# Kernel optimization log

Measured on AMD Instinct MI355X. Metric: run time of the kernel, lower is better.

Reference implementation:

```python
import jax, jax.numpy as jnp
import numpy as np

B, T, D = 2048, 200, 64
H1, H2 = 128, 64
NEG_INF = jnp.float32(-(2.0**32) + 1.0)


def setup_inputs() -> dict:
    key = jax.random.key(0)
    ks = jax.random.split(key, 10)
    query = jax.random.normal(ks[0], (B, D), dtype=jnp.float32)
    k = jax.random.normal(ks[1], (B, T, D), dtype=jnp.float32)
    v = jax.random.normal(ks[2], (B, T, D), dtype=jnp.float32)
    mask = jax.random.randint(ks[3], (B, T), 0, 2, dtype=jnp.int32)
    # Deep_layer params: concat width 4*D -> H1 -> H2 -> 1
    s1 = 1.0 / np.sqrt(4 * D)
    s2 = 1.0 / np.sqrt(H1)
    s3 = 1.0 / np.sqrt(H2)
    W1 = jax.random.normal(ks[4], (4 * D, H1), dtype=jnp.float32) * s1
    b1 = jnp.zeros((H1,), dtype=jnp.float32)
    W2 = jax.random.normal(ks[5], (H1, H2), dtype=jnp.float32) * s2
    b2 = jnp.zeros((H2,), dtype=jnp.float32)
    Wo = jax.random.normal(ks[6], (H2, 1), dtype=jnp.float32) * s3
    bo = jnp.zeros((1,), dtype=jnp.float32)
    return {"query": query, "key": k, "value": v, "mask": mask,
            "W1": W1, "b1": b1, "W2": W2, "b2": b2, "Wo": Wo, "bo": bo}


def reference(query, key, value, mask, W1, b1, W2, b2, Wo, bo):
    b, t, d = key.shape
    q = jnp.broadcast_to(query[:, None, :], (b, t, d))          # tile query over T
    emb = jnp.concatenate([q, key, q - key, q * key], axis=-1)  # [B,T,4D]
    h = jax.nn.relu(jnp.einsum('btf,fh->bth', emb, W1) + b1)    # [B,T,H1]
    h = jax.nn.relu(jnp.einsum('bth,hk->btk', h, W2) + b2)      # [B,T,H2]
    score = (jnp.einsum('btk,ko->bto', h, Wo) + bo)[..., 0]     # [B,T]
    score = jnp.where(mask == 0, NEG_INF, score)
    attn = jax.nn.softmax(score, axis=-1)                       # [B,T]
    out = jnp.einsum('bt,btd->bd', attn, value)                 # [B,D]
    return out
```

## Files before the change

### kernel.cpp

```cpp
#include <hip/hip_runtime.h>
#include <hip/hip_bf16.h>
#include <cstdint>
#include <cstddef>

#define NB 2048
#define NT 200
#define ND 64
#define NH1 128
#define NH2 64
#define NTILES 7
#define NTP 224

typedef __bf16 bf16x8 __attribute__((ext_vector_type(8)));
typedef float f32x4 __attribute__((ext_vector_type(4)));

#define MFMA16(A, Bv, C) __builtin_amdgcn_mfma_f32_16x16x32_bf16((A), (Bv), (C), 0, 0, 0)

union BF8u { __bf16 b[8]; bf16x8 v; uint4 u4; };

template<int N>
__device__ __forceinline__ float row_ror_add(float v) {
    int r = __builtin_amdgcn_update_dpp(0, __builtin_bit_cast(int, v),
                                        0x120 | N, 0xF, 0xF, false);
    return v + __builtin_bit_cast(float, r);
}

__global__ void prep_kernel(const float* __restrict__ W1, const float* __restrict__ W2,
                            float* __restrict__ Qp, float* __restrict__ AbT,
                            float* __restrict__ PT, __bf16* __restrict__ W2t) {
    int tid = blockIdx.x * blockDim.x + threadIdx.x;
    if (tid < 64 * NH1) {
        int c = tid >> 7, j = tid & 127;
        Qp[tid] = W1[c * NH1 + j] + W1[(128 + c) * NH1 + j];
        int jj = tid >> 6, cc = tid & 63;
        AbT[tid] = W1[(64 + cc) * NH1 + jj] - W1[(128 + cc) * NH1 + jj];
        PT[tid]  = W1[(192 + cc) * NH1 + jj];
        int j2 = tid >> 7, k = tid & 127;
        W2t[tid] = (__bf16)W2[k * NH2 + j2];
    }
}

__global__ __launch_bounds__(256, 4)
void attn_main(const float* __restrict__ query, const float* __restrict__ key,
               const float* __restrict__ value, const int* __restrict__ mask,
               const float* __restrict__ b1, const float* __restrict__ b2,
               const float* __restrict__ Wo,
               const float* __restrict__ Qp, const float* __restrict__ AbT,
               const float* __restrict__ PT, const __bf16* __restrict__ W2t,
               float* __restrict__ out)
{
    __shared__ __align__(16) char smem[30976];
    auto KHI0 = (__bf16(*)[72])(smem);
    auto KHI1 = (__bf16(*)[72])(smem + 4608);
    auto H10  = (__bf16(*)[136])(smem + 9216);
    auto H11  = (__bf16(*)[136])(smem + 17920);
    auto SP   = (float(*)[NTP])(smem + 26624);
    float* QS  = (float*)(smem + 30208);
    float* QHS = (float*)(smem + 30464);
    float* SCORES = (float*)(smem);
    auto REDS = (float(*)[72])(smem + 9216);

    const int b = blockIdx.x;
    const int tid = threadIdx.x;
    const int lane = tid & 63;
    const int wave = tid >> 6;
    const int jn = lane & 15;
    const int g4 = lane >> 4;
    const int g8 = g4 * 8;

    const int r_st = tid >> 3;
    const int c0   = (tid & 7) * 8;
    const float* kp_base = key + (size_t)b * NT * ND + c0;
    float4 pf0, pf1;

    auto load_tile = [&](int t0) {
        int t = t0 + r_st;
        t = t < NT ? t : NT - 1;
        const float* kp = kp_base + (size_t)t * ND;
        pf0 = *(const float4*)(kp);
        pf1 = *(const float4*)(kp + 4);
    };

    load_tile(0);

    if (tid < ND) QS[tid] = query[(size_t)b * ND + tid];
    int mk = 0;
    if (tid < NT) mk = mask[(size_t)b * NT + tid];
    __syncthreads();

    if (tid < NH1) {
        float a = b1[tid];
        #pragma unroll 8
        for (int c = 0; c < ND; ++c) a = fmaf(QS[c], Qp[c * NH1 + tid], a);
        QHS[tid] = a;
    }

    bf16x8 g1_bhi[2][2], g1_blo[2][2];
    const int jown = wave * 32;
    #pragma unroll
    for (int n = 0; n < 2; ++n) {
        const int j = jown + n * 16 + jn;
        #pragma unroll
        for (int kk = 0; kk < 2; ++kk) {
            const float* ab = AbT + j * ND + kk * 32 + g8;
            const float* pt = PT  + j * ND + kk * 32 + g8;
            float4 a0 = *(const float4*)ab, a1 = *(const float4*)(ab + 4);
            float4 p0 = *(const float4*)pt, p1 = *(const float4*)(pt + 4);
            const float va[8] = {a0.x,a0.y,a0.z,a0.w,a1.x,a1.y,a1.z,a1.w};
            const float vp[8] = {p0.x,p0.y,p0.z,p0.w,p1.x,p1.y,p1.z,p1.w};
            BF8u vh, vl;
            #pragma unroll
            for (int e = 0; e < 8; ++e) {
                const int c = kk * 32 + g8 + e;
                float v = fmaf(QS[c], vp[e], va[e]);
                __bf16 hi = (__bf16)v;
                vh.b[e] = hi;
                vl.b[e] = (__bf16)(v - (float)hi);
            }
            g1_bhi[n][kk] = vh.v;
            g1_blo[n][kk] = vl.v;
        }
    }
    bf16x8 g2_w[4];
    {
        const int j2 = wave * 16 + jn;
        #pragma unroll
        for (int kk = 0; kk < 4; ++kk)
            g2_w[kk] = *(const bf16x8*)(W2t + j2 * NH1 + kk * 32 + g8);
    }
    __syncthreads();
    const float qh0 = QHS[jown + jn];
    const float qh1 = QHS[jown + 16 + jn];
    const float b2j = b2[wave * 16 + jn];
    const float woj = Wo[wave * 16 + jn];

    f32x4 accc[2][2];
    for (int ti = 0; ti <= NTILES; ++ti) {
        __bf16 (*KCUR)[72]   = (ti & 1) ? KHI1 : KHI0;
        __bf16 (*H1CUR)[136] = ((ti - 1) & 1) ? H11 : H10;

        if (ti < NTILES) {
            const float vals[8] = {pf0.x, pf0.y, pf0.z, pf0.w, pf1.x, pf1.y, pf1.z, pf1.w};
            BF8u ph;
            #pragma unroll
            for (int i = 0; i < 8; ++i) ph.b[i] = (__bf16)vals[i];
            *(uint4*)(&KCUR[r_st][c0]) = ph.u4;
        }
        if (ti > 0) {
            #pragma unroll
            for (int mt = 0; mt < 2; ++mt)
            #pragma unroll
            for (int n = 0; n < 2; ++n) {
                const float qhj = n ? qh1 : qh0;
                const int j = jown + n * 16 + jn;
                #pragma unroll
                for (int r = 0; r < 4; ++r)
                    H1CUR[mt * 16 + g4 * 4 + r][j] =
                        (__bf16)fmaxf(accc[mt][n][r] + qhj, 0.f);
            }
        }
        __syncthreads();

        if (ti + 1 < NTILES) load_tile((ti + 1) * 32);

        if (ti < NTILES) {
            #pragma unroll
            for (int mt = 0; mt < 2; ++mt) {
                const int arow = mt * 16 + jn;
                const bf16x8 a0 = *(const bf16x8*)(&KCUR[arow][g8]);
                const bf16x8 a1 = *(const bf16x8*)(&KCUR[arow][32 + g8]);
                #pragma unroll
                for (int n = 0; n < 2; ++n) {
                    f32x4 ac = {0.f, 0.f, 0.f, 0.f};
                    ac = MFMA16(a0, g1_bhi[n][0], ac);
                    ac = MFMA16(a1, g1_bhi[n][1], ac);
                    ac = MFMA16(a0, g1_blo[n][0], ac);
                    ac = MFMA16(a1, g1_blo[n][1], ac);
                    accc[mt][n] = ac;
                }
            }
        }
        if (ti > 0) {
            const int t0 = (ti - 1) * 32;
            #pragma unroll
            for (int mt = 0; mt < 2; ++mt) {
                const int arow = mt * 16 + jn;
                const bf16x8 h0v = *(const bf16x8*)(&H1CUR[arow][g8]);
                const bf16x8 h1v = *(const bf16x8*)(&H1CUR[arow][32 + g8]);
                const bf16x8 h2v = *(const bf16x8*)(&H1CUR[arow][64 + g8]);
                const bf16x8 h3v = *(const bf16x8*)(&H1CUR[arow][96 + g8]);
                f32x4 cA = {0.f,0.f,0.f,0.f}, cB = {0.f,0.f,0.f,0.f};
                cA = MFMA16(h0v, g2_w[0], cA);
                cB = MFMA16(h1v, g2_w[1], cB);
                cA = MFMA16(h2v, g2_w[2], cA);
                cB = MFMA16(h3v, g2_w[3], cB);
                #pragma unroll
                for (int r = 0; r < 4; ++r) {
                    float v = fmaxf(cA[r] + cB[r] + b2j, 0.f) * woj;
                    v = row_ror_add<8>(v);
                    v = row_ror_add<4>(v);
                    v = row_ror_add<2>(v);
                    v = row_ror_add<1>(v);
                    if (jn == 0) SP[wave][t0 + mt * 16 + g4 * 4 + r] = v;
                }
            }
        }
    }
    __syncthreads();

    if (tid < NTP) {
        const float sc = SP[0][tid] + SP[1][tid] + SP[2][tid] + SP[3][tid];
        SCORES[tid] = (tid < NT && mk != 0) ? __expf(sc) : 0.f;
    }
    __syncthreads();

    {
        const int tg = tid >> 4;
        const int dq = tid & 15;
        const float* vbase = value + (size_t)b * NT * ND + dq * 4;
        float oa0 = 0.f, oa1 = 0.f, oa2 = 0.f, oa3 = 0.f, den = 0.f;
        for (int t = tg; t < NT; t += 16) {
            const float e = SCORES[t];
            const float4 v4 = *(const float4*)(vbase + (size_t)t * ND);
            oa0 = fmaf(e, v4.x, oa0); oa1 = fmaf(e, v4.y, oa1);
            oa2 = fmaf(e, v4.z, oa2); oa3 = fmaf(e, v4.w, oa3);
            den += e;
        }
        REDS[tg][dq*4+0] = oa0; REDS[tg][dq*4+1] = oa1;
        REDS[tg][dq*4+2] = oa2; REDS[tg][dq*4+3] = oa3;
        if (dq == 0) REDS[tg][64] = den;
    }
    __syncthreads();

    if (tid < ND) {
        float s = 0.f, den = 0.f;
        #pragma unroll
        for (int g = 0; g < 16; ++g) { s += REDS[g][tid]; den += REDS[g][64]; }
        out[(size_t)b * ND + tid] = s / den;
    }
}

extern "C" void kernel_launch(void* const* d_in, const int* in_sizes, int n_in,
                              void* d_out, int out_size, void* d_ws, size_t ws_size,
                              hipStream_t stream) {
    const float* query = (const float*)d_in[0];
    const float* key   = (const float*)d_in[1];
    const float* value = (const float*)d_in[2];
    const int*   maskp = (const int*)d_in[3];
    const float* W1    = (const float*)d_in[4];
    const float* b1    = (const float*)d_in[5];
    const float* W2    = (const float*)d_in[6];
    const float* b2    = (const float*)d_in[7];
    const float* Wo    = (const float*)d_in[8];
    float* out = (float*)d_out;

    float* Qp  = (float*)d_ws;
    float* AbT = Qp + 64 * NH1;
    float* PT  = AbT + NH1 * ND;
    __bf16* W2t = (__bf16*)(PT + NH1 * ND);

    prep_kernel<<<32, 256, 0, stream>>>(W1, W2, Qp, AbT, PT, W2t);
    attn_main<<<NB, 256, 0, stream>>>(query, key, value, maskp, b1, b2, Wo,
                                      Qp, AbT, PT, W2t, out);
}
```

Measured before the change: 61.74 us.

## Deepen key prefetch to two tiles, prefetch value early, use lightweight barriers

Key tiles are now prefetched two iterations ahead into a double-buffered register array, and the tile loop is fully unrolled. The first value rows are loaded before the score barrier so their latency overlaps the softmax step. __syncthreads is replaced by a barrier that waits only on LDS counters, occupancy is raised to 5 blocks per CU, and the query-projection dot product is split into four accumulators. The extra prefetch registers compete with the higher occupancy target and may cause spills.

```diff
diff --git a/kernel.cpp b/kernel.cpp
--- a/kernel.cpp
+++ b/kernel.cpp
@@ -23,6 +23,13 @@
     int r = __builtin_amdgcn_update_dpp(0, __builtin_bit_cast(int, v),
                                         0x120 | N, 0xF, 0xF, false);
     return v + __builtin_bit_cast(float, r);
+}
+
+__device__ __forceinline__ void bar_sync() {
+    __builtin_amdgcn_sched_barrier(0);
+    asm volatile("s_waitcnt lgkmcnt(0)" ::: "memory");
+    __builtin_amdgcn_s_barrier();
+    __builtin_amdgcn_sched_barrier(0);
 }
 
 __global__ void prep_kernel(const float* __restrict__ W1, const float* __restrict__ W2,
@@ -40,7 +47,7 @@
     }
 }
 
-__global__ __launch_bounds__(256, 4)
+__global__ __launch_bounds__(256, 5)
 void attn_main(const float* __restrict__ query, const float* __restrict__ key,
                const float* __restrict__ value, const int* __restrict__ mask,
                const float* __restrict__ b1, const float* __restrict__ b2,
@@ -71,28 +78,34 @@
     const int r_st = tid >> 3;
     const int c0   = (tid & 7) * 8;
     const float* kp_base = key + (size_t)b * NT * ND + c0;
-    float4 pf0, pf1;
-
-    auto load_tile = [&](int t0) {
-        int t = t0 + r_st;
-        t = t < NT ? t : NT - 1;
-        const float* kp = kp_base + (size_t)t * ND;
-        pf0 = *(const float4*)(kp);
-        pf1 = *(const float4*)(kp + 4);
-    };
-
-    load_tile(0);
+    float4 pf[2][2];
+
+    {
+        int t0 = r_st;
+        const float* kp0 = kp_base + (size_t)t0 * ND;
+        pf[0][0] = *(const float4*)(kp0);
+        pf[0][1] = *(const float4*)(kp0 + 4);
+        int t1 = 32 + r_st;
+        const float* kp1 = kp_base + (size_t)t1 * ND;
+        pf[1][0] = *(const float4*)(kp1);
+        pf[1][1] = *(const float4*)(kp1 + 4);
+    }
 
     if (tid < ND) QS[tid] = query[(size_t)b * ND + tid];
     int mk = 0;
     if (tid < NT) mk = mask[(size_t)b * NT + tid];
-    __syncthreads();
+    bar_sync();
 
     if (tid < NH1) {
-        float a = b1[tid];
-        #pragma unroll 8
-        for (int c = 0; c < ND; ++c) a = fmaf(QS[c], Qp[c * NH1 + tid], a);
-        QHS[tid] = a;
+        float a0 = 0.f, a1 = 0.f, a2 = 0.f, a3 = 0.f;
+        #pragma unroll
+        for (int c = 0; c < ND; c += 4) {
+            a0 = fmaf(QS[c],     Qp[c * NH1 + tid],       a0);
+            a1 = fmaf(QS[c + 1], Qp[(c + 1) * NH1 + tid], a1);
+            a2 = fmaf(QS[c + 2], Qp[(c + 2) * NH1 + tid], a2);
+            a3 = fmaf(QS[c + 3], Qp[(c + 3) * NH1 + tid], a3);
+        }
+        QHS[tid] = b1[tid] + ((a0 + a1) + (a2 + a3));
     }
 
     bf16x8 g1_bhi[2][2], g1_blo[2][2];
@@ -128,19 +141,22 @@
         for (int kk = 0; kk < 4; ++kk)
             g2_w[kk] = *(const bf16x8*)(W2t + j2 * NH1 + kk * 32 + g8);
     }
-    __syncthreads();
+    bar_sync();
     const float qh0 = QHS[jown + jn];
     const float qh1 = QHS[jown + 16 + jn];
     const float b2j = b2[wave * 16 + jn];
     const float woj = Wo[wave * 16 + jn];
 
     f32x4 accc[2][2];
+    #pragma unroll
     for (int ti = 0; ti <= NTILES; ++ti) {
         __bf16 (*KCUR)[72]   = (ti & 1) ? KHI1 : KHI0;
-        __bf16 (*H1CUR)[136] = ((ti - 1) & 1) ? H11 : H10;
+        __bf16 (*H1CUR)[136] = ((ti + 1) & 1) ? H11 : H10;
 
         if (ti < NTILES) {
-            const float vals[8] = {pf0.x, pf0.y, pf0.z, pf0.w, pf1.x, pf1.y, pf1.z, pf1.w};
+            const int bi = ti & 1;
+            const float vals[8] = {pf[bi][0].x, pf[bi][0].y, pf[bi][0].z, pf[bi][0].w,
+                                   pf[bi][1].x, pf[bi][1].y, pf[bi][1].z, pf[bi][1].w};
             BF8u ph;
             #pragma unroll
             for (int i = 0; i < 8; ++i) ph.b[i] = (__bf16)vals[i];
@@ -159,10 +175,16 @@
                         (__bf16)fmaxf(accc[mt][n][r] + qhj, 0.f);
             }
         }
-        __syncthreads();
-
-        if (ti + 1 < NTILES) load_tile((ti + 1) * 32);
-
+        bar_sync();
+
+        if (ti + 2 < NTILES) {
+            const int bi = ti & 1;
+            int t = (ti + 2) * 32 + r_st;
+            t = t < NT ? t : NT - 1;
+            const float* kp = kp_base + (size_t)t * ND;
+            pf[bi][0] = *(const float4*)(kp);
+            pf[bi][1] = *(const float4*)(kp + 4);
+        }
         if (ti < NTILES) {
             #pragma unroll
             for (int mt = 0; mt < 2; ++mt) {
@@ -206,20 +228,30 @@
             }
         }
     }
-    __syncthreads();
+
+    const int tg = tid >> 4;
+    const int dq = tid & 15;
+    const float* vbase = value + (size_t)b * NT * ND + dq * 4;
+    const float4 vv0 = *(const float4*)(vbase + (size_t)tg * ND);
+    const float4 vv1 = *(const float4*)(vbase + (size_t)(tg + 16) * ND);
+
+    bar_sync();
 
     if (tid < NTP) {
         const float sc = SP[0][tid] + SP[1][tid] + SP[2][tid] + SP[3][tid];
         SCORES[tid] = (tid < NT && mk != 0) ? __expf(sc) : 0.f;
     }
-    __syncthreads();
+    bar_sync();
 
     {
-        const int tg = tid >> 4;
-        const int dq = tid & 15;
-        const float* vbase = value + (size_t)b * NT * ND + dq * 4;
-        float oa0 = 0.f, oa1 = 0.f, oa2 = 0.f, oa3 = 0.f, den = 0.f;
-        for (int t = tg; t < NT; t += 16) {
+        const float e0 = SCORES[tg], e1 = SCORES[tg + 16];
+        float oa0 = fmaf(e1, vv1.x, e0 * vv0.x);
+        float oa1 = fmaf(e1, vv1.y, e0 * vv0.y);
+        float oa2 = fmaf(e1, vv1.z, e0 * vv0.z);
+        float oa3 = fmaf(e1, vv1.w, e0 * vv0.w);
+        float den = e0 + e1;
+        #pragma unroll 4
+        for (int t = tg + 32; t < NT; t += 16) {
             const float e = SCORES[t];
             const float4 v4 = *(const float4*)(vbase + (size_t)t * ND);
             oa0 = fmaf(e, v4.x, oa0); oa1 = fmaf(e, v4.y, oa1);
@@ -230,7 +262,7 @@
         REDS[tg][dq*4+2] = oa2; REDS[tg][dq*4+3] = oa3;
         if (dq == 0) REDS[tg][64] = den;
     }
-    __syncthreads();
+    bar_sync();
 
     if (tid < ND) {
         float s = 0.f, den = 0.f;
```

Result: slower. 90.43 us (+46.5%).
